# Kernel optimization log

Measured on AMD Instinct MI355X. Metric: run time of the kernel, lower is better.

Reference implementation:

```python
import jax, jax.numpy as jnp
import numpy as np

R = 16
ALPHA = 32.0
SCALING = ALPHA / max(1, R)

def setup_inputs() -> dict:
    key = jax.random.key(0)
    ks = jax.random.split(key, 7)
    B_, D, M = 16384, 1024, 4096
    return {
        "x": jax.random.normal(ks[0], (B_, D), dtype=jnp.float32),
        "W0": jax.random.normal(ks[1], (M, D), dtype=jnp.float32) * 0.02,
        "b0": jax.random.normal(ks[2], (M,), dtype=jnp.float32) * 0.02,
        "A": jax.random.normal(ks[3], (R, D), dtype=jnp.float32) * 0.001,
        "B": jax.random.normal(ks[4], (M, R), dtype=jnp.float32) * 0.02,
        "W2": jax.random.normal(ks[5], (1, M), dtype=jnp.float32) * 0.02,
        "b2": jax.random.normal(ks[6], (1,), dtype=jnp.float32) * 0.02,
    }

def reference(x, W0, b0, A, B, W2, b2):
    # effective_W = W0 + scaling * (B @ A)  -> [m_hidden, d_in]
    W_eff = W0 + SCALING * (B @ A)
    # F.linear(x, W_eff, b0): x @ W_eff^T + b0 -> [batch, m_hidden]
    h = jax.nn.relu(jnp.einsum('bd,md->bm', x, W_eff) + b0)
    # fc2: [batch, 1] then squeeze(-1)
    out = (jnp.einsum('bm,om->bo', h, W2) + b2).squeeze(-1)
    return out
```

## Files before the change

### kernel.cpp

```cpp
#include <hip/hip_runtime.h>
#include <hip/hip_bf16.h>
#include <stdint.h>

#define BATCH  16384
#define D_IN   1024
#define M_HID  4096
#define R_LORA 16
#define SCALING 2.0f

#define STRIP    64
#define NTHREADS 512

typedef __bf16 bf16x8 __attribute__((ext_vector_type(8)));
typedef float  f32x16 __attribute__((ext_vector_type(16)));

__device__ __forceinline__ unsigned short f2bf(float f) {
    union { float f; unsigned int u; } c; c.f = f;
    unsigned int u = c.u;
    return (unsigned short)((u + 0x7FFFu + ((u >> 16) & 1u)) >> 16);
}

__global__ __launch_bounds__(256) void k_wprep(
    const float* __restrict__ W0, const float* __restrict__ A,
    const float* __restrict__ Bl, unsigned short* __restrict__ wb)
{
    int id = blockIdx.x * 256 + threadIdx.x;
    int rl  = id & 31;
    int c   = (id >> 5) & 127;
    int n32 = id >> 12;
    int n = n32 * 32 + rl, k0 = c * 8;
    const float* wr = W0 + (size_t)n * D_IN + k0;
    float4 v0 = *(const float4*)(wr);
    float4 v1 = *(const float4*)(wr + 4);
    const float* brow = Bl + n * R_LORA;
#pragma unroll
    for (int r = 0; r < R_LORA; ++r) {
        float s = SCALING * brow[r];
        const float* ar = A + r * D_IN + k0;
        float4 a0 = *(const float4*)(ar);
        float4 a1 = *(const float4*)(ar + 4);
        v0.x += s * a0.x; v0.y += s * a0.y; v0.z += s * a0.z; v0.w += s * a0.w;
        v1.x += s * a1.x; v1.y += s * a1.y; v1.z += s * a1.z; v1.w += s * a1.w;
    }
    uint4 o;
    o.x = (unsigned)f2bf(v0.x) | ((unsigned)f2bf(v0.y) << 16);
    o.y = (unsigned)f2bf(v0.z) | ((unsigned)f2bf(v0.w) << 16);
    o.z = (unsigned)f2bf(v1.x) | ((unsigned)f2bf(v1.y) << 16);
    o.w = (unsigned)f2bf(v1.z) | ((unsigned)f2bf(v1.w) << 16);
    ((uint4*)wb)[id] = o;
}

__global__ __launch_bounds__(NTHREADS, 2) void k_strip(
    const float* __restrict__ xf, const unsigned short* __restrict__ wb,
    const float* __restrict__ b0, const float* __restrict__ W2,
    const float* __restrict__ b2, float* __restrict__ out)
{
    __shared__ unsigned short As[STRIP * D_IN];
    __shared__ float red[8][STRIP];

    const int tid  = threadIdx.x;
    const int lane = tid & 63;
    const int wave = tid >> 6;
    const int rl   = lane & 31;
    const int half = lane >> 5;
    const int row0 = blockIdx.x * STRIP;

    {
        const int r  = tid >> 3;
        const int c0 = tid & 7;
        const float* xr = xf + (size_t)(row0 + r) * D_IN;
#pragma unroll
        for (int i = 0; i < 16; ++i) {
            int c = i * 8 + c0;
            float4 v0 = *(const float4*)(xr + c * 8);
            float4 v1 = *(const float4*)(xr + c * 8 + 4);
            uint4 o;
            o.x = (unsigned)f2bf(v0.x) | ((unsigned)f2bf(v0.y) << 16);
            o.y = (unsigned)f2bf(v0.z) | ((unsigned)f2bf(v0.w) << 16);
            o.z = (unsigned)f2bf(v1.x) | ((unsigned)f2bf(v1.y) << 16);
            o.w = (unsigned)f2bf(v1.z) | ((unsigned)f2bf(v1.w) << 16);
            *(uint4*)(&As[c * 512 + r * 8]) = o;
        }
    }
    __syncthreads();

    float rowpart[2][16];
#pragma unroll
    for (int ti = 0; ti < 2; ++ti)
#pragma unroll
        for (int r = 0; r < 16; ++r) rowpart[ti][r] = 0.f;

    for (int pass = 0; pass < 8; ++pass) {
        const int n0 = wave * 64 + pass * 512;
        const float w2a = W2[n0 + rl],      b0a = b0[n0 + rl];
        const float w2b = W2[n0 + 32 + rl], b0b = b0[n0 + 32 + rl];
        const int n32 = wave * 2 + pass * 16;
        const unsigned short* w0p = wb + (size_t)n32 * 32768 + half * 256 + rl * 8;
        const unsigned short* w1p = w0p + 32768;

        f32x16 acc[2][2] = {};
        bf16x8 wf0[4], wf1[4];
#pragma unroll
        for (int p = 0; p < 4; ++p) {
            wf0[p] = *(const bf16x8*)(w0p + p * 512);
            wf1[p] = *(const bf16x8*)(w1p + p * 512);
        }

#pragma unroll 4
        for (int kk = 0; kk < 64; ++kk) {
            const int cur = kk & 3;
            const int coff = (kk * 2 + half) * 512 + rl * 8;
            bf16x8 af0 = *(const bf16x8*)(&As[coff]);
            bf16x8 af1 = *(const bf16x8*)(&As[coff + 256]);
            bf16x8 w0c = wf0[cur], w1c = wf1[cur];
            if (kk < 60) {
                wf0[cur] = *(const bf16x8*)(w0p + (kk + 4) * 512);
                wf1[cur] = *(const bf16x8*)(w1p + (kk + 4) * 512);
            }
            acc[0][0] = __builtin_amdgcn_mfma_f32_32x32x16_bf16(af0, w0c, acc[0][0], 0, 0, 0);
            acc[0][1] = __builtin_amdgcn_mfma_f32_32x32x16_bf16(af0, w1c, acc[0][1], 0, 0, 0);
            acc[1][0] = __builtin_amdgcn_mfma_f32_32x32x16_bf16(af1, w0c, acc[1][0], 0, 0, 0);
            acc[1][1] = __builtin_amdgcn_mfma_f32_32x32x16_bf16(af1, w1c, acc[1][1], 0, 0, 0);
        }

#pragma unroll
        for (int ti = 0; ti < 2; ++ti)
#pragma unroll
            for (int r = 0; r < 16; ++r)
                rowpart[ti][r] += fmaxf(acc[ti][0][r] + b0a, 0.f) * w2a
                                + fmaxf(acc[ti][1][r] + b0b, 0.f) * w2b;
    }

#pragma unroll
    for (int ti = 0; ti < 2; ++ti)
#pragma unroll
        for (int r = 0; r < 16; ++r) {
            float p = rowpart[ti][r];
#pragma unroll
            for (int m = 1; m <= 16; m <<= 1)
                p += __shfl_xor(p, m, 64);
            if (rl == 0)
                red[wave][ti * 32 + (r & 3) + 8 * (r >> 2) + 4 * half] = p;
        }
    __syncthreads();
    if (tid < STRIP) {
        float s = b2[0];
#pragma unroll
        for (int w = 0; w < 8; ++w) s += red[w][tid];
        out[row0 + tid] = s;
    }
}

__global__ __launch_bounds__(256) void k_naive(
    const float* __restrict__ x, const float* __restrict__ W0,
    const float* __restrict__ b0, const float* __restrict__ A,
    const float* __restrict__ Bl, const float* __restrict__ W2,
    const float* __restrict__ b2, float* __restrict__ out)
{
    __shared__ float xs[D_IN];
    int b = blockIdx.x;
    for (int d = threadIdx.x; d < D_IN; d += 256) xs[d] = x[(size_t)b * D_IN + d];
    __syncthreads();
    float part = 0.f;
    for (int m = threadIdx.x; m < M_HID; m += 256) {
        float h = b0[m];
        const float* wr = W0 + (size_t)m * D_IN;
        const float* brow = Bl + m * R_LORA;
        for (int d = 0; d < D_IN; ++d) {
            float w = wr[d];
            for (int r = 0; r < R_LORA; ++r) w += SCALING * brow[r] * A[r * D_IN + d];
            h += xs[d] * w;
        }
        part += fmaxf(h, 0.f) * W2[m];
    }
    __shared__ float sred[256];
    sred[threadIdx.x] = part;
    __syncthreads();
    for (int s = 128; s > 0; s >>= 1) {
        if (threadIdx.x < s) sred[threadIdx.x] += sred[threadIdx.x + s];
        __syncthreads();
    }
    if (threadIdx.x == 0) out[b] = sred[0] + b2[0];
}

extern "C" void kernel_launch(void* const* d_in, const int* in_sizes, int n_in,
                              void* d_out, int out_size, void* d_ws, size_t ws_size,
                              hipStream_t stream) {
    const float* x  = (const float*)d_in[0];
    const float* W0 = (const float*)d_in[1];
    const float* b0 = (const float*)d_in[2];
    const float* A  = (const float*)d_in[3];
    const float* Bl = (const float*)d_in[4];
    const float* W2 = (const float*)d_in[5];
    const float* b2 = (const float*)d_in[6];
    float* out = (float*)d_out;

    const size_t wb_bytes = (size_t)M_HID * D_IN * 2;
    if (ws_size >= wb_bytes) {
        unsigned short* wb = (unsigned short*)d_ws;
        hipLaunchKernelGGL(k_wprep, dim3(M_HID * D_IN / 8 / 256), dim3(256), 0, stream,
                           W0, A, Bl, wb);
        hipLaunchKernelGGL(k_strip, dim3(BATCH / STRIP), dim3(NTHREADS), 0, stream,
                           x, wb, b0, W2, b2, out);
    } else {
        hipLaunchKernelGGL(k_naive, dim3(BATCH), dim3(256), 0, stream,
                           x, W0, b0, A, Bl, W2, b2, out);
    }
}
```

Measured before the change: 248.5 us.

## Restructure weight-prep kernel to cache LoRA A in registers and transpose via LDS

```diff
diff --git a/kernel.cpp b/kernel.cpp
--- a/kernel.cpp
+++ b/kernel.cpp
@@ -24,30 +24,40 @@
     const float* __restrict__ W0, const float* __restrict__ A,
     const float* __restrict__ Bl, unsigned short* __restrict__ wb)
 {
-    int id = blockIdx.x * 256 + threadIdx.x;
-    int rl  = id & 31;
-    int c   = (id >> 5) & 127;
-    int n32 = id >> 12;
-    int n = n32 * 32 + rl, k0 = c * 8;
-    const float* wr = W0 + (size_t)n * D_IN + k0;
-    float4 v0 = *(const float4*)(wr);
-    float4 v1 = *(const float4*)(wr + 4);
-    const float* brow = Bl + n * R_LORA;
-#pragma unroll
-    for (int r = 0; r < R_LORA; ++r) {
-        float s = SCALING * brow[r];
-        const float* ar = A + r * D_IN + k0;
-        float4 a0 = *(const float4*)(ar);
-        float4 a1 = *(const float4*)(ar + 4);
-        v0.x += s * a0.x; v0.y += s * a0.y; v0.z += s * a0.z; v0.w += s * a0.w;
-        v1.x += s * a1.x; v1.y += s * a1.y; v1.z += s * a1.z; v1.w += s * a1.w;
-    }
-    uint4 o;
-    o.x = (unsigned)f2bf(v0.x) | ((unsigned)f2bf(v0.y) << 16);
-    o.y = (unsigned)f2bf(v0.z) | ((unsigned)f2bf(v0.w) << 16);
-    o.z = (unsigned)f2bf(v1.x) | ((unsigned)f2bf(v1.y) << 16);
-    o.w = (unsigned)f2bf(v1.z) | ((unsigned)f2bf(v1.w) << 16);
-    ((uint4*)wb)[id] = o;
+    __shared__ unsigned short T[32][D_IN + 8];
+    const int n32 = blockIdx.x;
+    const int t   = threadIdx.x;
+
+    float4 Areg[R_LORA];
+#pragma unroll
+    for (int j = 0; j < R_LORA; ++j)
+        Areg[j] = *(const float4*)(A + j * D_IN + t * 4);
+
+#pragma unroll 4
+    for (int r = 0; r < 32; ++r) {
+        const int n = n32 * 32 + r;
+        float4 v = *(const float4*)(W0 + (size_t)n * D_IN + t * 4);
+        const float* brow = Bl + n * R_LORA;
+#pragma unroll
+        for (int j = 0; j < R_LORA; ++j) {
+            float s = SCALING * brow[j];
+            v.x += s * Areg[j].x; v.y += s * Areg[j].y;
+            v.z += s * Areg[j].z; v.w += s * Areg[j].w;
+        }
+        ushort4 o = make_ushort4(f2bf(v.x), f2bf(v.y), f2bf(v.z), f2bf(v.w));
+        *(ushort4*)(&T[r][t * 4]) = o;
+    }
+    __syncthreads();
+
+    unsigned short* dst = wb + (size_t)n32 * 32768;
+#pragma unroll
+    for (int i = 0; i < 16; ++i) {
+        int L  = t * 128 + i * 8;
+        int c  = L >> 8;
+        int rl = (L >> 3) & 31;
+        uint4 v = *(const uint4*)(&T[rl][c * 8]);
+        *(uint4*)(dst + L) = v;
+    }
 }
 
 __global__ __launch_bounds__(NTHREADS, 2) void k_strip(
@@ -198,7 +208,7 @@
     const size_t wb_bytes = (size_t)M_HID * D_IN * 2;
     if (ws_size >= wb_bytes) {
         unsigned short* wb = (unsigned short*)d_ws;
-        hipLaunchKernelGGL(k_wprep, dim3(M_HID * D_IN / 8 / 256), dim3(256), 0, stream,
+        hipLaunchKernelGGL(k_wprep, dim3(M_HID / 32), dim3(256), 0, stream,
                            W0, A, Bl, wb);
         hipLaunchKernelGGL(k_strip, dim3(BATCH / STRIP), dim3(NTHREADS), 0, stream,
                            x, wb, b0, W2, b2, out);
```

After: 249.4 us. No clear change (+0.4%).
